# Kernel optimization log

Measured on AMD Instinct MI355X. Metric: run time of the kernel, lower is better.

The kernel has to match this reference:

```python
import jax, jax.numpy as jnp
import numpy as np

N = 100000   # n_nodes (= ninput, identity features)
E = 1600000  # edges per adjacency (avg degree 16)
H = 128      # nhid
EPS = 1e-12


def setup_inputs() -> dict:
    key = jax.random.key(0)
    ks = jax.random.split(key, 24)
    inp = {
        'adj1_rows': jax.random.randint(ks[0], (E,), 0, N),
        'adj1_cols': jax.random.randint(ks[1], (E,), 0, N),
        'adj1_vals': jax.random.uniform(ks[2], (E,), jnp.float32) / 16.0,
        'adj2_rows': jax.random.randint(ks[3], (E,), 0, N),
        'adj2_cols': jax.random.randint(ks[4], (E,), 0, N),
        'adj2_vals': jax.random.uniform(ks[5], (E,), jnp.float32) / 16.0,
    }
    s = 1.0 / np.sqrt(H)
    inp['w1'] = jax.random.uniform(ks[6], (N, H), jnp.float32, -s, s)
    for i in range(2, 10):
        inp[f'w{i}'] = jax.random.uniform(ks[5 + i], (H, H), jnp.float32, -s, s)
    s2 = 1.0 / np.sqrt(2 * H)
    inp['m1'] = jax.random.uniform(ks[15], (H, 2 * H), jnp.float32, -s, s)
    inp['b1'] = jnp.zeros((2 * H,), jnp.float32)
    inp['m2'] = jax.random.uniform(ks[16], (2 * H, 2 * H), jnp.float32, -s2, s2)
    inp['b2'] = jnp.zeros((2 * H,), jnp.float32)
    inp['m3'] = jax.random.uniform(ks[17], (2 * H, 1), jnp.float32, -s2, s2)
    inp['b3'] = jnp.zeros((1,), jnp.float32)
    return inp


def _spmm(rows, cols, vals, x):
    # sparse [N,N] @ dense [N,H] via gather + segment_sum
    return jax.ops.segment_sum(vals[:, None] * x[cols], rows, num_segments=N)


def _l2norm(x):
    # F.normalize(x, p=2, dim=1)
    n = jnp.sqrt(jnp.sum(x * x, axis=1, keepdims=True))
    return x / jnp.maximum(n, EPS)


def _mlp(x, m1, b1, m2, b2, m3, b3):
    # dropout inactive (eval mode) for deterministic reference
    h = jax.nn.relu(x @ m1 + b1)
    h = jax.nn.relu(h @ m2 + b2)
    return h @ m3 + b3  # [N,1]


def _branch(rows, cols, vals, w1, ws, mlp_params):
    x = jax.nn.relu(_spmm(rows, cols, vals, w1))
    x = _l2norm(x)
    score = _mlp(x, *mlp_params)
    for i, w in enumerate(ws):
        x = jax.nn.relu(_spmm(rows, cols, vals, x @ w))
        if i < len(ws) - 1:  # last layer (gc9) is relu only, no normalize
            x = _l2norm(x)
        score = score + _mlp(x, *mlp_params)
    return score


def reference(adj1_rows, adj1_cols, adj1_vals, adj2_rows, adj2_cols, adj2_vals,
              w1, w2, w3, w4, w5, w6, w7, w8, w9,
              m1, b1, m2, b2, m3, b3):
    ws = [w2, w3, w4, w5, w6, w7, w8, w9]
    mlp_params = (m1, b1, m2, b2, m3, b3)
    score1 = _branch(adj1_rows, adj1_cols, adj1_vals, w1, ws, mlp_params)
    score2 = _branch(adj2_rows, adj2_cols, adj2_vals, w1, ws, mlp_params)
    return score1 * score2  # [N,1]
```

## Files before the change

### kernel.cpp

```cpp
#include <hip/hip_runtime.h>
#include <hip/hip_fp16.h>

#define NN 100000
#define NE 1600000
#define HD 128
#define HD2 256

#define NBK 512
#define RPB 196
#define CH  4096
#define CAP 4096

typedef unsigned int u32;
typedef unsigned short u16;
typedef _Float16 half8 __attribute__((ext_vector_type(8)));
typedef float floatx4 __attribute__((ext_vector_type(4)));

static inline int cdiv(int a, int b){ return (a + b - 1) / b; }

__device__ __forceinline__ u32 split_pack(float v){
  __half h;
  if(fabsf(v) < 6.103515625e-05f) h = __ushort_as_half((u16)0);
  else h = __float2half_rn(v);
  float hf = __half2float(h);
  __half l = __float2half_rn((v - hf) * 4096.0f);
  return (u32)__half_as_ushort(h) | ((u32)__half_as_ushort(l) << 16);
}

__global__ void k_zero_f(float* __restrict__ p, int n){
  int i = blockIdx.x * 256 + threadIdx.x;
  if(i < n) p[i] = 0.f;
}

__global__ void k_init_bcap(int* __restrict__ bcur){
  int i = blockIdx.x * 256 + threadIdx.x;
  if(i < 2 * NBK) bcur[i] = (i & (NBK - 1)) * CAP;
}

__global__ void k_binscatter(const int* __restrict__ r0a, const int* __restrict__ c0a,
                             const float* __restrict__ v0a,
                             const int* __restrict__ r1a, const int* __restrict__ c1a,
                             const float* __restrict__ v1a,
                             int* __restrict__ bcur,
                             u32* __restrict__ sr0, uint2* __restrict__ sv0,
                             u32* __restrict__ sr1, uint2* __restrict__ sv1){
  __shared__ int cnt[NBK];
  __shared__ int bstart[NBK];
  __shared__ int gbase[NBK];
  __shared__ int sh[256];
  __shared__ u32 srow[CH];
  __shared__ uint2 scvs[CH];
  int z = blockIdx.y;
  const int* rows = z ? r1a : r0a;
  const int* cols = z ? c1a : c0a;
  const float* vals = z ? v1a : v0a;
  int* cur = bcur + z * NBK;
  u32* osr = z ? sr1 : sr0;
  uint2* osv = z ? sv1 : sv0;
  int t = threadIdx.x;
  for(int i = t; i < NBK; i += 256) cnt[i] = 0;
  __syncthreads();
  int e0 = blockIdx.x * CH;
  int total = NE - e0; if(total > CH) total = CH;
  int r_[16], c_[16], b_[16], k_[16]; float v_[16];
  #pragma unroll
  for(int k = 0; k < 16; k++){
    int e = e0 + t + k * 256;
    b_[k] = -1;
    if(e < NE){
      r_[k] = rows[e]; c_[k] = cols[e]; v_[k] = vals[e];
      b_[k] = r_[k] / RPB;
      k_[k] = atomicAdd(&cnt[b_[k]], 1);
    }
  }
  __syncthreads();
  int v0 = cnt[2 * t], v1 = cnt[2 * t + 1];
  int s2 = v0 + v1;
  sh[t] = s2;
  __syncthreads();
  for(int d = 1; d < 256; d <<= 1){
    int tv = (t >= d) ? sh[t - d] : 0;
    __syncthreads();
    sh[t] += tv;
    __syncthreads();
  }
  int excl = sh[t] - s2;
  bstart[2 * t] = excl;
  bstart[2 * t + 1] = excl + v0;
  __syncthreads();
  #pragma unroll
  for(int k = 0; k < 16; k++){
    if(b_[k] >= 0){
      int slot = bstart[b_[k]] + k_[k];
      srow[slot] = (u32)r_[k];
      scvs[slot] = make_uint2((u32)c_[k], __float_as_uint(v_[k]));
    }
  }
  for(int b = t; b < NBK; b += 256){
    int c = cnt[b];
    if(c > 0) gbase[b] = atomicAdd(&cur[b], c);
  }
  __syncthreads();
  for(int i = t; i < total; i += 256){
    u32 r = srow[i];
    int b = (int)r / RPB;
    int dest = gbase[b] + (i - bstart[b]);
    osr[dest] = r;
    osv[dest] = scvs[i];
  }
}

__global__ void k_bucket_scan(const int* __restrict__ bcur, int* __restrict__ bbase,
                              int* __restrict__ c1ptr, int* __restrict__ c2ptr){
  __shared__ int sh[256];
  int z = blockIdx.x;
  const int* cur = bcur + z * NBK;
  int* bb = bbase + z * NBK;
  int t = threadIdx.x;
  int v0 = cur[2 * t]     - (2 * t) * CAP;
  int v1 = cur[2 * t + 1] - (2 * t + 1) * CAP;
  int s2 = v0 + v1;
  sh[t] = s2;
  __syncthreads();
  for(int d = 1; d < 256; d <<= 1){
    int tv = (t >= d) ? sh[t - d] : 0;
    __syncthreads();
    sh[t] += tv;
    __syncthreads();
  }
  int excl = sh[t] - s2;
  bb[2 * t] = excl;
  bb[2 * t + 1] = excl + v0;
  if(t == 0){
    int* rp = z ? c2ptr : c1ptr;
    rp[NN] = NE;
  }
}

__global__ void k_bucket_place(const int* __restrict__ bcur, const int* __restrict__ bbase,
                               const u32* __restrict__ sr0, const uint2* __restrict__ sv0,
                               const u32* __restrict__ sr1, const uint2* __restrict__ sv1,
                               int* __restrict__ c1ptr, int* __restrict__ c2ptr,
                               uint2* __restrict__ e0, uint2* __restrict__ e1){
  __shared__ int hist[RPB];
  __shared__ int cur[RPB];
  __shared__ int sh[256];
  __shared__ u32 srows[CAP];
  int z = blockIdx.y;
  int b = blockIdx.x;
  int r0 = b * RPB;
  if(r0 >= NN) return;
  int rend = r0 + RPB; if(rend > NN) rend = NN;
  int nr = rend - r0;
  const u32* sr = z ? sr1 : sr0;
  const uint2* sv = z ? sv1 : sv0;
  int* rp = z ? c2ptr : c1ptr;
  uint2* ecv = z ? e1 : e0;
  int cnt = bcur[z * NBK + b] - b * CAP;
  int base = bbase[z * NBK + b];
  int g = b * CAP;
  int t = threadIdx.x;
  for(int r = t; r < nr; r += 256) hist[r] = 0;
  __syncthreads();
  for(int i = t; i < cnt; i += 256){
    u32 r = sr[g + i];
    srows[i] = r;
    atomicAdd(&hist[(int)r - r0], 1);
  }
  __syncthreads();
  int v = (t < nr) ? hist[t] : 0;
  sh[t] = v;
  __syncthreads();
  for(int d = 1; d < 256; d <<= 1){
    int tv = (t >= d) ? sh[t - d] : 0;
    __syncthreads();
    sh[t] += tv;
    __syncthreads();
  }
  int excl = sh[t] - v;
  if(t < nr){
    rp[r0 + t] = base + excl;
    cur[t] = base + excl;
  }
  __syncthreads();
  for(int i = t; i < cnt; i += 256){
    int r = (int)srows[i] - r0;
    int p = atomicAdd(&cur[r], 1);
    ecv[p] = sv[g + i];
  }
}

__global__ void k_splitw(const float* __restrict__ W, u32* __restrict__ out,
                         int K, int N, int total){
  int idx = blockIdx.x * 256 + threadIdx.x;
  if(idx < total){
    int n = idx / K, k = idx - n * K;
    out[idx] = split_pack(W[(size_t)k * N + n]);
  }
}

template<bool NORM>
__global__ void k_spmm(const int* __restrict__ rowptr, const uint2* __restrict__ ecv,
                       const float* __restrict__ X, u32* __restrict__ outpk){
  int node = (blockIdx.x << 2) + (threadIdx.x >> 6);
  int lane = threadIdx.x & 63;
  if(node >= NN) return;
  int s = rowptr[node], e = rowptr[node + 1];
  float ax = 0.f, ay = 0.f, bx = 0.f, by = 0.f;
  int i = s;
  for(; i + 15 < e; i += 16){
    uint2 ee[16]; float2 xx[16];
    #pragma unroll
    for(int j = 0; j < 16; j++) ee[j] = ecv[i + j];
    #pragma unroll
    for(int j = 0; j < 16; j++) xx[j] = *(const float2*)(X + (size_t)ee[j].x * HD + lane * 2);
    #pragma unroll
    for(int j = 0; j < 16; j += 4){
      ax += __uint_as_float(ee[j].y)   * xx[j].x   + __uint_as_float(ee[j+1].y) * xx[j+1].x;
      ay += __uint_as_float(ee[j].y)   * xx[j].y   + __uint_as_float(ee[j+1].y) * xx[j+1].y;
      bx += __uint_as_float(ee[j+2].y) * xx[j+2].x + __uint_as_float(ee[j+3].y) * xx[j+3].x;
      by += __uint_as_float(ee[j+2].y) * xx[j+2].y + __uint_as_float(ee[j+3].y) * xx[j+3].y;
    }
  }
  for(; i + 3 < e; i += 4){
    uint2 f0 = ecv[i], f1 = ecv[i+1], f2 = ecv[i+2], f3 = ecv[i+3];
    float2 x0 = *(const float2*)(X + (size_t)f0.x * HD + lane * 2);
    float2 x1 = *(const float2*)(X + (size_t)f1.x * HD + lane * 2);
    float2 x2 = *(const float2*)(X + (size_t)f2.x * HD + lane * 2);
    float2 x3 = *(const float2*)(X + (size_t)f3.x * HD + lane * 2);
    ax += __uint_as_float(f0.y) * x0.x + __uint_as_float(f1.y) * x1.x;
    ay += __uint_as_float(f0.y) * x0.y + __uint_as_float(f1.y) * x1.y;
    bx += __uint_as_float(f2.y) * x2.x + __uint_as_float(f3.y) * x3.x;
    by += __uint_as_float(f2.y) * x2.y + __uint_as_float(f3.y) * x3.y;
  }
  for(; i < e; i++){
    uint2 f0 = ecv[i];
    float2 xv = *(const float2*)(X + (size_t)f0.x * HD + lane * 2);
    ax += __uint_as_float(f0.y) * xv.x;
    ay += __uint_as_float(f0.y) * xv.y;
  }
  ax += bx; ay += by;
  ax = fmaxf(ax, 0.f);
  ay = fmaxf(ay, 0.f);
  if(NORM){
    float ss = ax * ax + ay * ay;
    #pragma unroll
    for(int o = 32; o >= 1; o >>= 1) ss += __shfl_xor(ss, o, 64);
    float scale = 1.f / fmaxf(sqrtf(ss), 1e-12f);
    ax *= scale; ay *= scale;
  }
  *(uint2*)(outpk + (size_t)node * HD + lane * 2) = make_uint2(split_pack(ax), split_pack(ay));
}

template<int MODE>
__launch_bounds__(256, 2)
__global__ void k_mfma_gemm(const u32* __restrict__ Apk, const u32* __restrict__ Btpk,
                            const u32* __restrict__ Bt1pk,
                            const float* __restrict__ bias, float* __restrict__ Yout,
                            u32* __restrict__ Hout, const float* __restrict__ m3,
                            float* __restrict__ score, int M, int K, int N){
  __shared__ u16 As_h[128 * 40], As_l[128 * 40];
  __shared__ u16 Bs_h[128 * 40], Bs_l[128 * 40];
  constexpr int NYC = (MODE == 0) ? 1 : ((MODE == 3) ? 3 : 2);
  const int d = blockIdx.x;
  const int grp = d / (8 * NYC);
  const int rem = d - grp * 8 * NYC;
  const int rt = grp * 8 + (rem & 7);
  const int ct = rem >> 3;
  const int nrt = (M + 127) >> 7;
  if(rt >= nrt) return;
  const int tid = threadIdx.x;
  const int lane = tid & 63, wid = tid >> 6;
  const int lm = lane & 15, lg = lane >> 4;
  const int mq = (wid & 1) * 64, nq = (wid >> 1) * 64;
  const int m0 = rt * 128;
  int n0 = ct * 128;
  const u32* Bt = Btpk;
  bool m0path = true;
  if(MODE == 3){
    m0path = (ct == 0);
    if(m0path){ n0 = 0; }
    else      { n0 = (ct - 1) * 128; Bt = Bt1pk; }
  }

  floatx4 accA[4][4], accB[4][4];
  #pragma unroll
  for(int i = 0; i < 4; i++)
    #pragma unroll
    for(int j = 0; j < 4; j++){
      accA[i][j] = (floatx4){0.f, 0.f, 0.f, 0.f};
      accB[i][j] = (floatx4){0.f, 0.f, 0.f, 0.f};
    }

  for(int k0 = 0; k0 < K; k0 += 32){
    uint4 av[4], bv[4];
    #pragma unroll
    for(int j = 0; j < 4; j++){
      int li = tid + j * 256;
      int row = li >> 3, kc = (li & 7) * 4;
      int ar = m0 + row; if(ar >= M) ar = M - 1;
      av[j] = *(const uint4*)(Apk + (size_t)ar * K + k0 + kc);
      bv[j] = *(const uint4*)(Bt + (size_t)(n0 + row) * K + k0 + kc);
    }
    if(k0) __syncthreads();
    #pragma unroll
    for(int j = 0; j < 4; j++){
      int li = tid + j * 256;
      int row = li >> 3, kc = (li & 7) * 4;
      int base = row * 40 + kc;
      ushort4 h, l;
      h.x = (u16)(av[j].x & 0xffff); l.x = (u16)(av[j].x >> 16);
      h.y = (u16)(av[j].y & 0xffff); l.y = (u16)(av[j].y >> 16);
      h.z = (u16)(av[j].z & 0xffff); l.z = (u16)(av[j].z >> 16);
      h.w = (u16)(av[j].w & 0xffff); l.w = (u16)(av[j].w >> 16);
      *(ushort4*)&As_h[base] = h;
      *(ushort4*)&As_l[base] = l;
      h.x = (u16)(bv[j].x & 0xffff); l.x = (u16)(bv[j].x >> 16);
      h.y = (u16)(bv[j].y & 0xffff); l.y = (u16)(bv[j].y >> 16);
      h.z = (u16)(bv[j].z & 0xffff); l.z = (u16)(bv[j].z >> 16);
      h.w = (u16)(bv[j].w & 0xffff); l.w = (u16)(bv[j].w >> 16);
      *(ushort4*)&Bs_h[base] = h;
      *(ushort4*)&Bs_l[base] = l;
    }
    __syncthreads();

    half8 fa_h[4], fa_l[4], fb_h[4], fb_l[4];
    #pragma unroll
    for(int s = 0; s < 4; s++){
      int ra = (mq + s * 16 + lm) * 40 + lg * 8;
      fa_h[s] = *(const half8*)&As_h[ra];
      fa_l[s] = *(const half8*)&As_l[ra];
      int rb = (nq + s * 16 + lm) * 40 + lg * 8;
      fb_h[s] = *(const half8*)&Bs_h[rb];
      fb_l[s] = *(const half8*)&Bs_l[rb];
    }
    #pragma unroll
    for(int i = 0; i < 4; i++)
      #pragma unroll
      for(int j = 0; j < 4; j++){
        accA[i][j] = __builtin_amdgcn_mfma_f32_16x16x32_f16(fa_h[i], fb_h[j], accA[i][j], 0, 0, 0);
        accB[i][j] = __builtin_amdgcn_mfma_f32_16x16x32_f16(fa_h[i], fb_l[j], accB[i][j], 0, 0, 0);
        accB[i][j] = __builtin_amdgcn_mfma_f32_16x16x32_f16(fa_l[i], fb_h[j], accB[i][j], 0, 0, 0);
      }
  }

  const float inv4096 = 1.f / 4096.f;
  if(MODE == 0 || (MODE == 3 && m0path)){
    int ldy = (MODE == 3) ? HD : N;
    #pragma unroll
    for(int i = 0; i < 4; i++)
      #pragma unroll
      for(int r = 0; r < 4; r++){
        int m = m0 + mq + i * 16 + lg * 4 + r;
        if(m < M){
          #pragma unroll
          for(int j = 0; j < 4; j++){
            int c = n0 + nq + j * 16 + lm;
            Yout[(size_t)m * ldy + c] = accA[i][j][r] + accB[i][j][r] * inv4096;
          }
        }
      }
  } else if(MODE == 1 || MODE == 3){
    int ldh = (MODE == 3) ? HD2 : N;
    #pragma unroll
    for(int i = 0; i < 4; i++)
      #pragma unroll
      for(int r = 0; r < 4; r++){
        int m = m0 + mq + i * 16 + lg * 4 + r;
        if(m < M){
          #pragma unroll
          for(int j = 0; j < 4; j++){
            int c = n0 + nq + j * 16 + lm;
            float v = fmaxf(accA[i][j][r] + accB[i][j][r] * inv4096 + bias[c], 0.f);
            Hout[(size_t)m * ldh + c] = split_pack(v);
          }
        }
      }
  } else {
    #pragma unroll
    for(int i = 0; i < 4; i++)
      #pragma unroll
      for(int r = 0; r < 4; r++){
        float s = 0.f;
        #pragma unroll
        for(int j = 0; j < 4; j++){
          int c = n0 + nq + j * 16 + lm;
          float v = fmaxf(accA[i][j][r] + accB[i][j][r] * inv4096 + bias[c], 0.f);
          s = fmaf(v, m3[c], s);
        }
        s += __shfl_xor(s, 1, 64);
        s += __shfl_xor(s, 2, 64);
        s += __shfl_xor(s, 4, 64);
        s += __shfl_xor(s, 8, 64);
        int m = m0 + mq + i * 16 + lg * 4 + r;
        if(lm == 0 && m < M) atomicAdd(&score[m], s);
      }
  }
}

__global__ void k_final(const float* __restrict__ sc, const float* __restrict__ b3,
                        float* __restrict__ out){
  int i = blockIdx.x * 256 + threadIdx.x;
  if(i < NN){
    float b = 9.f * b3[0];
    out[i] = (sc[i] + b) * (sc[NN + i] + b);
  }
}

extern "C" void kernel_launch(void* const* d_in, const int* in_sizes, int n_in,
                              void* d_out, int out_size, void* d_ws, size_t ws_size,
                              hipStream_t stream){
  const int*   a1r = (const int*)d_in[0];
  const int*   a1c = (const int*)d_in[1];
  const float* a1v = (const float*)d_in[2];
  const int*   a2r = (const int*)d_in[3];
  const int*   a2c = (const int*)d_in[4];
  const float* a2v = (const float*)d_in[5];
  const float* w1  = (const float*)d_in[6];
  const float* w[8];
  for(int i = 0; i < 8; i++) w[i] = (const float*)d_in[7 + i];
  const float* m1 = (const float*)d_in[15];
  const float* b1 = (const float*)d_in[16];
  const float* m2 = (const float*)d_in[17];
  const float* b2 = (const float*)d_in[18];
  const float* m3 = (const float*)d_in[19];
  const float* b3 = (const float*)d_in[20];
  float* out = (float*)d_out;

  char* base = (char*)d_ws;
  size_t off = 0;
  auto alloc = [&](size_t bytes) -> char* {
    char* r = base + off;
    off += (bytes + 255) & ~(size_t)255;
    return r;
  };
  int*   c1ptr = (int*)  alloc((size_t)(NN + 1) * 4);
  int*   c2ptr = (int*)  alloc((size_t)(NN + 1) * 4);
  uint2* ecv1  = (uint2*)alloc((size_t)NE * 8);
  uint2* ecv2  = (uint2*)alloc((size_t)NE * 8);
  int*   cursor= (int*)  alloc((size_t)2 * NBK * 4);
  int*   bbase = (int*)  alloc((size_t)2 * NBK * 4);
  float* sc    = (float*)alloc((size_t)2 * NN * 4);
  u32*   wtpk[8];
  for(int i = 0; i < 8; i++) wtpk[i] = (u32*)alloc((size_t)HD * HD * 4);
  u32*   m1tpk = (u32*)alloc((size_t)HD2 * HD * 4);
  u32*   m2tpk = (u32*)alloc((size_t)HD2 * HD2 * 4);
  u32*   xpk   = (u32*)alloc((size_t)NN * HD * 4);
  u32*   h1pk  = (u32*)alloc((size_t)NN * HD2 * 4);
  size_t need_ded = off + (((size_t)NN * HD * 4 + 255) & ~(size_t)255);
  bool ded_y = (ws_size >= need_ded);
  float* y = ded_y ? (float*)alloc((size_t)NN * HD * 4) : (float*)h1pk;

  const size_t SZ = (size_t)NBK * CAP;
  char* hb = (char*)h1pk;
  uint2* sv1 = (uint2*)hb;
  u32*   sr1 = (u32*)(hb + SZ * 8);
  uint2* sv2 = (uint2*)(hb + SZ * 12);
  u32*   sr2 = (u32*)(hb + SZ * 20);

  hipLaunchKernelGGL(k_init_bcap, dim3(cdiv(2 * NBK, 256)), dim3(256), 0, stream, cursor);
  hipLaunchKernelGGL(k_binscatter, dim3(cdiv(NE, CH), 2), dim3(256), 0, stream,
                     a1r, a1c, a1v, a2r, a2c, a2v, cursor, sr1, sv1, sr2, sv2);
  hipLaunchKernelGGL(k_bucket_scan, dim3(2), dim3(256), 0, stream, cursor, bbase, c1ptr, c2ptr);
  hipLaunchKernelGGL(k_bucket_place, dim3(NBK, 2), dim3(256), 0, stream,
                     cursor, bbase, sr1, sv1, sr2, sv2, c1ptr, c2ptr, ecv1, ecv2);

  auto splitw = [&](const float* W, u32* o, int K, int N){
    int total = K * N;
    hipLaunchKernelGGL(k_splitw, dim3(cdiv(total, 256)), dim3(256), 0, stream, W, o, K, N, total);
  };
  for(int i = 0; i < 8; i++) splitw(w[i], wtpk[i], HD, HD);
  splitw(m1, m1tpk, HD, HD2);
  splitw(m2, m2tpk, HD2, HD2);
  hipLaunchKernelGGL(k_zero_f, dim3(cdiv(2 * NN, 256)), dim3(256), 0, stream, sc, 2 * NN);

  const int NRT = cdiv(NN, 128);
  const int GP  = cdiv(NRT, 8) * 8;
  auto mode1 = [&](){
    hipLaunchKernelGGL((k_mfma_gemm<1>), dim3(GP * 2), dim3(256), 0, stream,
                       xpk, m1tpk, (const u32*)nullptr, b1, (float*)nullptr, h1pk,
                       (const float*)nullptr, (float*)nullptr, NN, HD, HD2);
  };
  auto mode2 = [&](float* score){
    hipLaunchKernelGGL((k_mfma_gemm<2>), dim3(GP * 2), dim3(256), 0, stream,
                       h1pk, m2tpk, (const u32*)nullptr, b2, (float*)nullptr, (u32*)nullptr,
                       m3, score, NN, HD2, HD2);
  };
  auto gemm0 = [&](int i){
    hipLaunchKernelGGL((k_mfma_gemm<0>), dim3(GP * 1), dim3(256), 0, stream,
                       xpk, wtpk[i], (const u32*)nullptr, (const float*)nullptr, y, (u32*)nullptr,
                       (const float*)nullptr, (float*)nullptr, NN, HD, HD);
  };
  auto fused01 = [&](int i){
    hipLaunchKernelGGL((k_mfma_gemm<3>), dim3(GP * 3), dim3(256), 0, stream,
                       xpk, wtpk[i], m1tpk, b1, y, h1pk,
                       (const float*)nullptr, (float*)nullptr, NN, HD, 0);
  };

  for(int b = 0; b < 2; b++){
    const int* rp = b ? c2ptr : c1ptr;
    const uint2* ecv = b ? ecv2 : ecv1;
    float* score = sc + (size_t)b * NN;
    hipLaunchKernelGGL((k_spmm<true>), dim3(cdiv(NN, 4)), dim3(256), 0, stream,
                       rp, ecv, w1, xpk);
    if(ded_y){
      for(int i = 0; i < 8; i++){
        fused01(i);
        mode2(score);
        if(i < 7)
          hipLaunchKernelGGL((k_spmm<true>),  dim3(cdiv(NN, 4)), dim3(256), 0, stream,
                             rp, ecv, y, xpk);
        else
          hipLaunchKernelGGL((k_spmm<false>), dim3(cdiv(NN, 4)), dim3(256), 0, stream,
                             rp, ecv, y, xpk);
      }
      mode1();
      mode2(score);
    } else {
      mode1();
      mode2(score);
      for(int i = 0; i < 8; i++){
        gemm0(i);
        if(i < 7)
          hipLaunchKernelGGL((k_spmm<true>),  dim3(cdiv(NN, 4)), dim3(256), 0, stream,
                             rp, ecv, y, xpk);
        else
          hipLaunchKernelGGL((k_spmm<false>), dim3(cdiv(NN, 4)), dim3(256), 0, stream,
                             rp, ecv, y, xpk);
        mode1();
        mode2(score);
      }
    }
  }

  hipLaunchKernelGGL(k_final, dim3(cdiv(NN, 256)), dim3(256), 0, stream, sc, b3, out);
}
```

Baseline: 4.282 ms.

## Co-schedule MLP second GEMM with next SpMM in one combined launch

Adds a combined kernel whose first blocks run the second MLP GEMM (scoring) and whose remaining blocks run the next layer's SpMM, since the two are independent. The first SpMM of branch 2 is also folded into the final scoring pair of branch 1. The aim is to overlap the compute-bound GEMM with the memory-bound gather and cut launch count. In exchange the SpMM blocks now carry the GEMM's shared-memory allocation and launch bounds, which may lower their occupancy.

```diff
diff --git a/kernel.cpp b/kernel.cpp
--- a/kernel.cpp
+++ b/kernel.cpp
@@ -200,9 +200,11 @@
 }
 
 template<bool NORM>
-__global__ void k_spmm(const int* __restrict__ rowptr, const uint2* __restrict__ ecv,
-                       const float* __restrict__ X, u32* __restrict__ outpk){
-  int node = (blockIdx.x << 2) + (threadIdx.x >> 6);
+__device__ __forceinline__ void dev_spmm(int vb, const int* __restrict__ rowptr,
+                                         const uint2* __restrict__ ecv,
+                                         const float* __restrict__ X,
+                                         u32* __restrict__ outpk){
+  int node = (vb << 2) + ((int)threadIdx.x >> 6);
   int lane = threadIdx.x & 63;
   if(node >= NN) return;
   int s = rowptr[node], e = rowptr[node + 1];
@@ -252,17 +254,21 @@
   *(uint2*)(outpk + (size_t)node * HD + lane * 2) = make_uint2(split_pack(ax), split_pack(ay));
 }
 
+template<bool NORM>
+__global__ void k_spmm(const int* __restrict__ rowptr, const uint2* __restrict__ ecv,
+                       const float* __restrict__ X, u32* __restrict__ outpk){
+  dev_spmm<NORM>(blockIdx.x, rowptr, ecv, X, outpk);
+}
+
 template<int MODE>
-__launch_bounds__(256, 2)
-__global__ void k_mfma_gemm(const u32* __restrict__ Apk, const u32* __restrict__ Btpk,
+__device__ __forceinline__ void dev_gemm(int d,
+                            const u32* __restrict__ Apk, const u32* __restrict__ Btpk,
                             const u32* __restrict__ Bt1pk,
                             const float* __restrict__ bias, float* __restrict__ Yout,
                             u32* __restrict__ Hout, const float* __restrict__ m3,
-                            float* __restrict__ score, int M, int K, int N){
-  __shared__ u16 As_h[128 * 40], As_l[128 * 40];
-  __shared__ u16 Bs_h[128 * 40], Bs_l[128 * 40];
+                            float* __restrict__ score, int M, int K, int N,
+                            u16* As_h, u16* As_l, u16* Bs_h, u16* Bs_l){
   constexpr int NYC = (MODE == 0) ? 1 : ((MODE == 3) ? 3 : 2);
-  const int d = blockIdx.x;
   const int grp = d / (8 * NYC);
   const int rem = d - grp * 8 * NYC;
   const int rt = grp * 8 + (rem & 7);
@@ -395,6 +401,36 @@
         int m = m0 + mq + i * 16 + lg * 4 + r;
         if(lm == 0 && m < M) atomicAdd(&score[m], s);
       }
+  }
+}
+
+template<int MODE>
+__launch_bounds__(256, 2)
+__global__ void k_mfma_gemm(const u32* __restrict__ Apk, const u32* __restrict__ Btpk,
+                            const u32* __restrict__ Bt1pk,
+                            const float* __restrict__ bias, float* __restrict__ Yout,
+                            u32* __restrict__ Hout, const float* __restrict__ m3,
+                            float* __restrict__ score, int M, int K, int N){
+  __shared__ u16 As_h[128 * 40], As_l[128 * 40];
+  __shared__ u16 Bs_h[128 * 40], Bs_l[128 * 40];
+  dev_gemm<MODE>(blockIdx.x, Apk, Btpk, Bt1pk, bias, Yout, Hout, m3, score,
+                 M, K, N, As_h, As_l, Bs_h, Bs_l);
+}
+
+template<bool NORM>
+__launch_bounds__(256, 2)
+__global__ void k_pair(const u32* __restrict__ Apk, const u32* __restrict__ Btpk,
+                       const float* __restrict__ bias, const float* __restrict__ m3,
+                       float* __restrict__ score, int gb,
+                       const int* __restrict__ rowptr, const uint2* __restrict__ ecv,
+                       const float* __restrict__ X, u32* __restrict__ outpk){
+  __shared__ u16 As_h[128 * 40], As_l[128 * 40];
+  __shared__ u16 Bs_h[128 * 40], Bs_l[128 * 40];
+  if((int)blockIdx.x < gb){
+    dev_gemm<2>(blockIdx.x, Apk, Btpk, (const u32*)nullptr, bias, (float*)nullptr,
+                (u32*)nullptr, m3, score, NN, HD2, HD2, As_h, As_l, Bs_h, Bs_l);
+  } else {
+    dev_spmm<NORM>((int)blockIdx.x - gb, rowptr, ecv, X, outpk);
   }
 }
 
@@ -476,6 +512,7 @@
 
   const int NRT = cdiv(NN, 128);
   const int GP  = cdiv(NRT, 8) * 8;
+  const int SPB = cdiv(NN, 4);
   auto mode1 = [&](){
     hipLaunchKernelGGL((k_mfma_gemm<1>), dim3(GP * 2), dim3(256), 0, stream,
                        xpk, m1tpk, (const u32*)nullptr, b1, (float*)nullptr, h1pk,
@@ -496,36 +533,49 @@
                        xpk, wtpk[i], m1tpk, b1, y, h1pk,
                        (const float*)nullptr, (float*)nullptr, NN, HD, 0);
   };
-
-  for(int b = 0; b < 2; b++){
-    const int* rp = b ? c2ptr : c1ptr;
-    const uint2* ecv = b ? ecv2 : ecv1;
-    float* score = sc + (size_t)b * NN;
-    hipLaunchKernelGGL((k_spmm<true>), dim3(cdiv(NN, 4)), dim3(256), 0, stream,
-                       rp, ecv, w1, xpk);
-    if(ded_y){
+  auto pair = [&](float* score, const int* rp, const uint2* ecv, const float* X, bool norm){
+    if(norm)
+      hipLaunchKernelGGL((k_pair<true>),  dim3(GP * 2 + SPB), dim3(256), 0, stream,
+                         h1pk, m2tpk, b2, m3, score, GP * 2, rp, ecv, X, xpk);
+    else
+      hipLaunchKernelGGL((k_pair<false>), dim3(GP * 2 + SPB), dim3(256), 0, stream,
+                         h1pk, m2tpk, b2, m3, score, GP * 2, rp, ecv, X, xpk);
+  };
+
+  if(ded_y){
+    hipLaunchKernelGGL((k_spmm<true>), dim3(SPB), dim3(256), 0, stream,
+                       c1ptr, ecv1, w1, xpk);
+    for(int b = 0; b < 2; b++){
+      const int* rp = b ? c2ptr : c1ptr;
+      const uint2* ecv = b ? ecv2 : ecv1;
+      float* score = sc + (size_t)b * NN;
       for(int i = 0; i < 8; i++){
         fused01(i);
+        pair(score, rp, ecv, y, i < 7);
+      }
+      mode1();
+      if(b == 0){
+        pair(score, c2ptr, ecv2, w1, true);
+      } else {
         mode2(score);
-        if(i < 7)
-          hipLaunchKernelGGL((k_spmm<true>),  dim3(cdiv(NN, 4)), dim3(256), 0, stream,
-                             rp, ecv, y, xpk);
-        else
-          hipLaunchKernelGGL((k_spmm<false>), dim3(cdiv(NN, 4)), dim3(256), 0, stream,
-                             rp, ecv, y, xpk);
-      }
-      mode1();
-      mode2(score);
-    } else {
+      }
+    }
+  } else {
+    for(int b = 0; b < 2; b++){
+      const int* rp = b ? c2ptr : c1ptr;
+      const uint2* ecv = b ? ecv2 : ecv1;
+      float* score = sc + (size_t)b * NN;
+      hipLaunchKernelGGL((k_spmm<true>), dim3(SPB), dim3(256), 0, stream,
+                         rp, ecv, w1, xpk);
       mode1();
       mode2(score);
       for(int i = 0; i < 8; i++){
         gemm0(i);
         if(i < 7)
-          hipLaunchKernelGGL((k_spmm<true>),  dim3(cdiv(NN, 4)), dim3(256), 0, stream,
+          hipLaunchKernelGGL((k_spmm<true>),  dim3(SPB), dim3(256), 0, stream,
                              rp, ecv, y, xpk);
         else
-          hipLaunchKernelGGL((k_spmm<false>), dim3(cdiv(NN, 4)), dim3(256), 0, stream,
+          hipLaunchKernelGGL((k_spmm<false>), dim3(SPB), dim3(256), 0, stream,
                              rp, ecv, y, xpk);
         mode1();
         mode2(score);
```

Result: slower. 5.683 ms (+32.7%).
